# Kernel optimization log

Hardware: AMD Instinct MI355X
Metric: run time of the kernel (lower is better)

## Reference

```python
import jax, jax.numpy as jnp
import numpy as np

WS = 7        # window_size
SHIFT = 3     # shift_size
HEADS = 12
EMBED = 384


def _relative_position_index(ws: int) -> np.ndarray:
    coords = np.stack(np.meshgrid(np.arange(ws), np.arange(ws), indexing='ij'))  # [2,ws,ws]
    flat = coords.reshape(2, -1)                                                 # [2,ws*ws]
    rel = flat[:, :, None] - flat[:, None, :]                                     # [2,N,N]
    rel = rel.transpose(1, 2, 0)
    rel[:, :, 0] += ws - 1
    rel[:, :, 1] += ws - 1
    rel[:, :, 0] *= 2 * ws - 1
    return rel.sum(-1)  # [ws*ws, ws*ws]


def setup_inputs() -> dict:
    key = jax.random.key(0)
    ks = jax.random.split(key, 6)
    B, H, W, C = 32, 56, 56, EMBED
    x = jax.random.normal(ks[0], (B, H * W, C), dtype=jnp.float32)
    s = 0.02
    qkv_w = jax.random.normal(ks[1], (C, 3 * C), dtype=jnp.float32) * s
    qkv_b = jnp.zeros((3 * C,), dtype=jnp.float32)
    proj_w = jax.random.normal(ks[2], (C, C), dtype=jnp.float32) * s
    proj_b = jnp.zeros((C,), dtype=jnp.float32)
    rel_bias_table = jax.random.normal(ks[3], ((2 * WS - 1) ** 2, HEADS), dtype=jnp.float32) * s
    return {"x": x, "qkv_w": qkv_w, "qkv_b": qkv_b, "proj_w": proj_w,
            "proj_b": proj_b, "rel_bias_table": rel_bias_table, "H": H, "W": W}


def reference(x, qkv_w, qkv_b, proj_w, proj_b, rel_bias_table, H, W):
    B, L, C = x.shape
    hd = C // HEADS
    scale = hd ** (-0.5)
    ws = WS
    x = x.reshape(B, H, W, C)
    # pad to multiples of window size (static python ints)
    pad_r = (ws - W % ws) % ws
    pad_b_ = (ws - H % ws) % ws
    if pad_r or pad_b_:
        x = jnp.pad(x, ((0, 0), (0, pad_b_), (0, pad_r), (0, 0)))
    Hp, Wp = H + pad_b_, W + pad_r
    # cyclic shift
    if SHIFT > 0:
        x = jnp.roll(x, shift=(-SHIFT, -SHIFT), axis=(1, 2))
    # window partition -> [nW, ws*ws, C]
    nh, nw = Hp // ws, Wp // ws
    xw = x.reshape(B, nh, ws, nw, ws, C).transpose(0, 1, 3, 2, 4, 5).reshape(-1, ws * ws, C)
    # qkv projection
    qkv = xw @ qkv_w + qkv_b                               # [nW, N, 3C]
    qkv = qkv.reshape(-1, ws * ws, 3, HEADS, hd).transpose(2, 0, 3, 1, 4)
    q, k, v = qkv[0], qkv[1], qkv[2]                        # [nW, heads, N, hd]
    attn = jnp.einsum('whnd,whmd->whnm', q, k) * scale
    rpi = jnp.asarray(_relative_position_index(ws))         # [N, N] static
    bias = rel_bias_table[rpi.reshape(-1)].reshape(ws * ws, ws * ws, HEADS)
    attn = attn + bias.transpose(2, 0, 1)[None]             # [1, heads, N, N]
    attn = jax.nn.softmax(attn, axis=-1)
    out = jnp.einsum('whnm,whmd->whnd', attn, v)            # [nW, heads, N, hd]
    out = out.transpose(0, 2, 1, 3).reshape(-1, ws, ws, C)
    # merge windows
    out = out.reshape(B, nh, nw, ws, ws, C).transpose(0, 1, 3, 2, 4, 5).reshape(B, Hp, Wp, C)
    if SHIFT > 0:
        out = jnp.roll(out, shift=(SHIFT, SHIFT), axis=(1, 2))
    if pad_r or pad_b_:
        out = out[:, :H, :W, :]
    out = out.reshape(B, H * W, C)
    return out @ proj_w + proj_b
```

## Files before the change

### kernel.cpp

```cpp
#include <hip/hip_runtime.h>


typedef __attribute__((ext_vector_type(8))) short short8;
typedef __attribute__((ext_vector_type(4))) float floatx4;

#define CDIM  384
#define QKVN  1152
#define MROWS 100352
#define LROW  3136

static constexpr size_t QKV_ELEMS = 38535168ull;
static constexpr size_t OFF_Q    = 0;
static constexpr size_t OFF_K    = OFF_Q  + QKV_ELEMS * 2 + 4096;
static constexpr size_t OFF_V    = OFF_K  + QKV_ELEMS * 2 + 4096;
static constexpr size_t OFF_AO   = OFF_V  + QKV_ELEMS * 2 + 4096;
static constexpr size_t OFF_WQ   = OFF_AO + (size_t)MROWS * CDIM * 2 + 4096;
static constexpr size_t OFF_WP   = OFF_WQ + (size_t)QKVN * CDIM * 2 + 256;
static constexpr size_t OFF_BIAS = OFF_WP + (size_t)CDIM * CDIM * 2 + 256;

__device__ __forceinline__ unsigned short f2bf(float f) {
  unsigned int u = __float_as_uint(f);
  unsigned int lsb = (u >> 16) & 1u;
  u += 0x7fffu + lsb;
  return (unsigned short)(u >> 16);
}

__device__ __forceinline__ void gl2lds16(const void* g, void* l) {
  __builtin_amdgcn_global_load_lds(
      (const __attribute__((address_space(1))) unsigned int*)g,
      (__attribute__((address_space(3))) unsigned int*)l, 16, 0, 0);
}

__global__ __launch_bounds__(256) void prep_kernel(
    const float* __restrict__ x, const float* __restrict__ qkv_w,
    const float* __restrict__ proj_w, const float* __restrict__ rbt,
    char* __restrict__ ws) {
  unsigned short* Wq = (unsigned short*)(ws + OFF_WQ);
  unsigned short* Wp = (unsigned short*)(ws + OFF_WP);
  unsigned short* XB = (unsigned short*)(ws + OFF_AO);
  float* biasp = (float*)(ws + OFF_BIAS);
  const int tid = blockIdx.x * blockDim.x + threadIdx.x;
  const int stride = gridDim.x * blockDim.x;
  for (int idx = tid; idx < QKVN * CDIM; idx += stride) {
    int n = idx / CDIM, k = idx - n * CDIM;
    Wq[idx] = f2bf(qkv_w[(size_t)k * QKVN + n]);
  }
  for (int idx = tid; idx < CDIM * CDIM; idx += stride) {
    int n = idx / CDIM, k = idx - n * CDIM;
    Wp[idx] = f2bf(proj_w[(size_t)k * CDIM + n]);
  }
  for (int idx = tid; idx < 12 * 64 * 64; idx += stride) {
    int h = idx / 4096;
    int rem = idx - h * 4096;
    int lane = rem / 64;
    int e = rem - lane * 64;
    int fm = e >> 4, fn = (e >> 2) & 3, r = e & 3;
    int row = fm * 16 + (lane >> 4) * 4 + r;
    int col = fn * 16 + (lane & 15);
    float v = -1e30f;
    if (row < 49 && col < 49) {
      int i = row / 7, j = row - i * 7;
      int k2 = col / 7, l2 = col - k2 * 7;
      int rpi = (i - k2 + 6) * 13 + (j - l2 + 6);
      v = rbt[rpi * 12 + h];
    }
    biasp[idx] = v;
  }
  const size_t n8 = (size_t)MROWS * CDIM / 8;
  for (size_t idx = tid; idx < n8; idx += stride) {
    const float4* s = (const float4*)(x + idx * 8);
    float4 f0 = s[0], f1 = s[1];
    uint4 o;
    o.x = (unsigned)f2bf(f0.x) | ((unsigned)f2bf(f0.y) << 16);
    o.y = (unsigned)f2bf(f0.z) | ((unsigned)f2bf(f0.w) << 16);
    o.z = (unsigned)f2bf(f1.x) | ((unsigned)f2bf(f1.y) << 16);
    o.w = (unsigned)f2bf(f1.z) | ((unsigned)f2bf(f1.w) << 16);
    ((uint4*)XB)[idx] = o;
  }
}

__global__ __launch_bounds__(256) void qkv_gemm(
    const float* __restrict__ qkv_b, char* __restrict__ ws) {
  __shared__ unsigned short As[128][32];
  __shared__ unsigned short Bs[128][32];
  const unsigned short* XB = (const unsigned short*)(ws + OFF_AO);
  const unsigned short* Wq = (const unsigned short*)(ws + OFF_WQ);
  unsigned short* Qb = (unsigned short*)(ws + OFF_Q);
  unsigned short* Kb = (unsigned short*)(ws + OFF_K);
  unsigned short* Vb = (unsigned short*)(ws + OFF_V);
  const int L = blockIdx.x;
  const int xcd = L & 7, slot = L >> 3;
  const int g9 = slot / 9;
  const int m0 = (g9 * 8 + xcd) * 128;
  const int n0 = (slot - g9 * 9) * 128;
  const int t = threadIdx.x;
  const int lane = t & 63, li = lane & 15, qd = lane >> 4;
  const int wv = t >> 6, wm = wv >> 1, wn = wv & 1;
  const int ld_r = lane >> 2;
  const int ld_c = (lane & 3) * 8;
  const unsigned short* agp = XB + (size_t)(m0 + wv * 32 + ld_r) * CDIM + ld_c;
  const unsigned short* bgp = Wq + (size_t)(n0 + wv * 32 + ld_r) * CDIM + ld_c;
  floatx4 acc[4][4] = {};
  for (int k0 = 0; k0 < CDIM; k0 += 32) {
    gl2lds16(agp + k0,             &As[wv * 32][0]);
    gl2lds16(agp + k0 + 16 * CDIM, &As[wv * 32 + 16][0]);
    gl2lds16(bgp + k0,             &Bs[wv * 32][0]);
    gl2lds16(bgp + k0 + 16 * CDIM, &Bs[wv * 32 + 16][0]);
    __syncthreads();
    short8 a[4], b[4];
#pragma unroll
    for (int f = 0; f < 4; f++)
      a[f] = *(const short8*)&As[wm * 64 + f * 16 + li][qd * 8];
#pragma unroll
    for (int f = 0; f < 4; f++)
      b[f] = *(const short8*)&Bs[wn * 64 + f * 16 + li][qd * 8];
#pragma unroll
    for (int i = 0; i < 4; i++)
#pragma unroll
      for (int j = 0; j < 4; j++)
        acc[i][j] = __builtin_amdgcn_mfma_f32_16x16x32_bf16(a[i], b[j], acc[i][j], 0, 0, 0);
    __syncthreads();
  }
  const int which = n0 / CDIM;
  unsigned short* dst = which == 0 ? Qb : (which == 1 ? Kb : Vb);
  const float mul = (which == 0) ? 0.17677669529663689f : 1.0f;
#pragma unroll
  for (int i = 0; i < 4; i++) {
    int winr[4], nidxr[4];
#pragma unroll
    for (int r = 0; r < 4; r++) {
      int m = m0 + wm * 64 + i * 16 + qd * 4 + r;
      int b_ = m / LROW, l = m - b_ * LROW;
      int y = l / 56, xx = l - y * 56;
      int yr = y + 53; if (yr >= 56) yr -= 56;
      int xr = xx + 53; if (xr >= 56) xr -= 56;
      winr[r] = b_ * 64 + (yr / 7) * 8 + (xr / 7);
      nidxr[r] = (yr % 7) * 7 + (xr % 7);
    }
#pragma unroll
    for (int j = 0; j < 4; j++) {
      int c = n0 + wn * 64 + j * 16 + li;
      int cc = c - which * CDIM;
      int head = cc >> 5, d = cc & 31;
      float bval = qkv_b[c];
#pragma unroll
      for (int r = 0; r < 4; r++) {
        size_t off = ((size_t)(winr[r] * 12 + head) * 49 + nidxr[r]) * 32 + d;
        dst[off] = f2bf((acc[i][j][r] + bval) * mul);
      }
    }
  }
}

__global__ __launch_bounds__(256) void attn_kernel(char* __restrict__ ws) {
  __shared__ unsigned short SMEM[4][64 * 72];
  const int win = blockIdx.x;
  const int t = threadIdx.x, wv = t >> 6, lane = t & 63;
  const int h = blockIdx.y * 4 + wv;
  const int li = lane & 15, qd = lane >> 4;
  unsigned short* Sm = &SMEM[wv][0];
  const size_t whoff = (size_t)(win * 12 + h) * 49 * 32;
  const unsigned short* Qb = (const unsigned short*)(ws + OFF_Q) + whoff;
  const unsigned short* Kb = (const unsigned short*)(ws + OFF_K) + whoff;
  const unsigned short* Vb = (const unsigned short*)(ws + OFF_V) + whoff;
  const float* biasp = (const float*)(ws + OFF_BIAS) + ((size_t)h * 64 + lane) * 64;

  {
    const uint2* vsrc = (const uint2*)Vb;
    for (int idx = lane; idx < 392; idx += 64) {
      uint2 d = vsrc[idx];
      unsigned short* p = Sm + (idx >> 3) * 34 + (idx & 7) * 4;
      *(unsigned int*)p = d.x;
      *(unsigned int*)(p + 2) = d.y;
    }
    for (int idx = lane; idx < 120; idx += 64) {
      unsigned short* p = Sm + (49 + (idx >> 3)) * 34 + (idx & 7) * 4;
      *(unsigned int*)p = 0;
      *(unsigned int*)(p + 2) = 0;
    }
  }

  short8 qa[4], kb4[4];
#pragma unroll
  for (int f = 0; f < 4; f++) {
    qa[f] = *(const short8*)(Qb + (f * 16 + li) * 32 + qd * 8);
    kb4[f] = *(const short8*)(Kb + (f * 16 + li) * 32 + qd * 8);
  }
  floatx4 s[4][4] = {};
#pragma unroll
  for (int i = 0; i < 4; i++)
#pragma unroll
    for (int j = 0; j < 4; j++)
      s[i][j] = __builtin_amdgcn_mfma_f32_16x16x32_bf16(qa[i], kb4[j], s[i][j], 0, 0, 0);

  short8 vb[2][2];
#pragma unroll
  for (int ss = 0; ss < 2; ss++)
#pragma unroll
    for (int nf = 0; nf < 2; nf++) {
      short8 tmp;
#pragma unroll
      for (int j = 0; j < 8; j++)
        tmp[j] = (short)Sm[(ss * 32 + qd * 8 + j) * 34 + nf * 16 + li];
      vb[ss][nf] = tmp;
    }

  float rsum[4][4];
#pragma unroll
  for (int fm = 0; fm < 4; fm++) {
#pragma unroll
    for (int fn = 0; fn < 4; fn++) {
      floatx4 bv = *(const floatx4*)(biasp + (fm * 4 + fn) * 4);
#pragma unroll
      for (int r = 0; r < 4; r++)
        s[fm][fn][r] = __expf(s[fm][fn][r] + bv[r]);
    }
#pragma unroll
    for (int r = 0; r < 4; r++) {
      float v = s[fm][0][r] + s[fm][1][r] + s[fm][2][r] + s[fm][3][r];
      v += __shfl_xor(v, 1);
      v += __shfl_xor(v, 2);
      v += __shfl_xor(v, 4);
      v += __shfl_xor(v, 8);
      rsum[fm][r] = v;
    }
#pragma unroll
    for (int fn = 0; fn < 4; fn++)
#pragma unroll
      for (int r = 0; r < 4; r++)
        Sm[(fm * 16 + qd * 4 + r) * 72 + fn * 16 + li] = f2bf(s[fm][fn][r]);
  }

  floatx4 o[4][2] = {};
#pragma unroll
  for (int fm = 0; fm < 4; fm++)
#pragma unroll
    for (int ss = 0; ss < 2; ss++) {
      short8 pa = *(const short8*)&Sm[(fm * 16 + li) * 72 + ss * 32 + qd * 8];
#pragma unroll
      for (int nf = 0; nf < 2; nf++)
        o[fm][nf] = __builtin_amdgcn_mfma_f32_16x16x32_bf16(pa, vb[ss][nf], o[fm][nf], 0, 0, 0);
    }

  unsigned short* AO = (unsigned short*)(ws + OFF_AO);
  const int b_ = win >> 6, wrem = win & 63, wy = wrem >> 3, wx = wrem & 7;
#pragma unroll
  for (int fm = 0; fm < 4; fm++)
#pragma unroll
    for (int r = 0; r < 4; r++) {
      int n = fm * 16 + qd * 4 + r;
      if (n >= 49) continue;
      float inv = 1.0f / rsum[fm][r];
      int i_ = n / 7, j_ = n - i_ * 7;
      int y = wy * 7 + i_ + 3;  if (y >= 56) y -= 56;
      int xx = wx * 7 + j_ + 3; if (xx >= 56) xx -= 56;
      size_t base = ((size_t)b_ * LROW + y * 56 + xx) * CDIM + h * 32;
#pragma unroll
      for (int nf = 0; nf < 2; nf++)
        AO[base + nf * 16 + li] = f2bf(o[fm][nf][r] * inv);
    }
}

__global__ __launch_bounds__(256) void proj_gemm(
    const float* __restrict__ proj_b, char* __restrict__ ws,
    float* __restrict__ out) {
  __shared__ unsigned short As[128][32];
  __shared__ unsigned short Bs[128][32];
  const unsigned short* AO = (const unsigned short*)(ws + OFF_AO);
  const unsigned short* Wp = (const unsigned short*)(ws + OFF_WP);
  const int L = blockIdx.x;
  const int xcd = L & 7, slot = L >> 3;
  const int g3 = slot / 3;
  const int m0 = (g3 * 8 + xcd) * 128;
  const int n0 = (slot - g3 * 3) * 128;
  const int t = threadIdx.x;
  const int lane = t & 63, li = lane & 15, qd = lane >> 4;
  const int wv = t >> 6, wm = wv >> 1, wn = wv & 1;
  const int ld_r = lane >> 2;
  const int ld_c = (lane & 3) * 8;
  const unsigned short* agp = AO + (size_t)(m0 + wv * 32 + ld_r) * CDIM + ld_c;
  const unsigned short* bgp = Wp + (size_t)(n0 + wv * 32 + ld_r) * CDIM + ld_c;
  floatx4 acc[4][4] = {};
  for (int k0 = 0; k0 < CDIM; k0 += 32) {
    gl2lds16(agp + k0,             &As[wv * 32][0]);
    gl2lds16(agp + k0 + 16 * CDIM, &As[wv * 32 + 16][0]);
    gl2lds16(bgp + k0,             &Bs[wv * 32][0]);
    gl2lds16(bgp + k0 + 16 * CDIM, &Bs[wv * 32 + 16][0]);
    __syncthreads();
    short8 a[4], b[4];
#pragma unroll
    for (int f = 0; f < 4; f++)
      a[f] = *(const short8*)&As[wm * 64 + f * 16 + li][qd * 8];
#pragma unroll
    for (int f = 0; f < 4; f++)
      b[f] = *(const short8*)&Bs[wn * 64 + f * 16 + li][qd * 8];
#pragma unroll
    for (int i = 0; i < 4; i++)
#pragma unroll
      for (int j = 0; j < 4; j++)
        acc[i][j] = __builtin_amdgcn_mfma_f32_16x16x32_bf16(a[i], b[j], acc[i][j], 0, 0, 0);
    __syncthreads();
  }
#pragma unroll
  for (int i = 0; i < 4; i++)
#pragma unroll
    for (int j = 0; j < 4; j++) {
      int c = n0 + wn * 64 + j * 16 + li;
      float bv = proj_b[c];
#pragma unroll
      for (int r = 0; r < 4; r++) {
        int m = m0 + wm * 64 + i * 16 + qd * 4 + r;
        out[(size_t)m * CDIM + c] = acc[i][j][r] + bv;
      }
    }
}

extern "C" void kernel_launch(void* const* d_in, const int* in_sizes, int n_in,
                              void* d_out, int out_size, void* d_ws, size_t ws_size,
                              hipStream_t stream) {
  const float* x      = (const float*)d_in[0];
  const float* qkv_w  = (const float*)d_in[1];
  const float* qkv_b  = (const float*)d_in[2];
  const float* proj_w = (const float*)d_in[3];
  const float* proj_b = (const float*)d_in[4];
  const float* rbt    = (const float*)d_in[5];
  char* ws = (char*)d_ws;
  float* out = (float*)d_out;

  prep_kernel<<<2048, 256, 0, stream>>>(x, qkv_w, proj_w, rbt, ws);
  qkv_gemm<<<7056, 256, 0, stream>>>(qkv_b, ws);
  attn_kernel<<<dim3(2048, 3), 256, 0, stream>>>(ws);
  proj_gemm<<<2352, 256, 0, stream>>>(proj_b, ws, out);
}
```

Before: 611.6 us.

## Double-buffer LDS tiles in both GEMMs and precompute window-scatter offsets

Both the QKV and projection GEMMs now use two LDS buffers and issue the global-to-LDS loads for the next K tile before computing the current one, so load latency can overlap MFMA work. A lookup table of per-row window scatter offsets is built in the prep kernel and read in the QKV epilogue, replacing the integer divides and mods. This doubles LDS use per block, which may lower occupancy. The global_load_lds writes are not waited on explicitly before the barrier, so correctness relies on the sync implying vmcnt drain.

```diff
diff --git a/kernel.cpp b/kernel.cpp
--- a/kernel.cpp
+++ b/kernel.cpp
@@ -17,6 +17,7 @@
 static constexpr size_t OFF_WQ   = OFF_AO + (size_t)MROWS * CDIM * 2 + 4096;
 static constexpr size_t OFF_WP   = OFF_WQ + (size_t)QKVN * CDIM * 2 + 256;
 static constexpr size_t OFF_BIAS = OFF_WP + (size_t)CDIM * CDIM * 2 + 256;
+static constexpr size_t OFF_LUT  = OFF_BIAS + (size_t)12 * 64 * 64 * 4 + 256;
 
 __device__ __forceinline__ unsigned short f2bf(float f) {
   unsigned int u = __float_as_uint(f);
@@ -39,6 +40,7 @@
   unsigned short* Wp = (unsigned short*)(ws + OFF_WP);
   unsigned short* XB = (unsigned short*)(ws + OFF_AO);
   float* biasp = (float*)(ws + OFF_BIAS);
+  int* lut = (int*)(ws + OFF_LUT);
   const int tid = blockIdx.x * blockDim.x + threadIdx.x;
   const int stride = gridDim.x * blockDim.x;
   for (int idx = tid; idx < QKVN * CDIM; idx += stride) {
@@ -66,6 +68,15 @@
     }
     biasp[idx] = v;
   }
+  for (int idx = tid; idx < MROWS; idx += stride) {
+    int b_ = idx / LROW, l = idx - b_ * LROW;
+    int y = l / 56, xx = l - y * 56;
+    int yr = y + 53; if (yr >= 56) yr -= 56;
+    int xr = xx + 53; if (xr >= 56) xr -= 56;
+    int win = b_ * 64 + (yr / 7) * 8 + (xr / 7);
+    int nidx = (yr % 7) * 7 + (xr % 7);
+    lut[idx] = win * 18816 + nidx * 32;
+  }
   const size_t n8 = (size_t)MROWS * CDIM / 8;
   for (size_t idx = tid; idx < n8; idx += stride) {
     const float4* s = (const float4*)(x + idx * 8);
@@ -81,13 +92,14 @@
 
 __global__ __launch_bounds__(256) void qkv_gemm(
     const float* __restrict__ qkv_b, char* __restrict__ ws) {
-  __shared__ unsigned short As[128][32];
-  __shared__ unsigned short Bs[128][32];
+  __shared__ unsigned short As[2][128][32];
+  __shared__ unsigned short Bs[2][128][32];
   const unsigned short* XB = (const unsigned short*)(ws + OFF_AO);
   const unsigned short* Wq = (const unsigned short*)(ws + OFF_WQ);
   unsigned short* Qb = (unsigned short*)(ws + OFF_Q);
   unsigned short* Kb = (unsigned short*)(ws + OFF_K);
   unsigned short* Vb = (unsigned short*)(ws + OFF_V);
+  const int* lut = (const int*)(ws + OFF_LUT);
   const int L = blockIdx.x;
   const int xcd = L & 7, slot = L >> 3;
   const int g9 = slot / 9;
@@ -100,20 +112,28 @@
   const int ld_c = (lane & 3) * 8;
   const unsigned short* agp = XB + (size_t)(m0 + wv * 32 + ld_r) * CDIM + ld_c;
   const unsigned short* bgp = Wq + (size_t)(n0 + wv * 32 + ld_r) * CDIM + ld_c;
+
+#define QSTAGE(buf, k0)                                          \
+  do {                                                           \
+    gl2lds16(agp + (k0),             &As[buf][wv * 32][0]);      \
+    gl2lds16(agp + (k0) + 16 * CDIM, &As[buf][wv * 32 + 16][0]); \
+    gl2lds16(bgp + (k0),             &Bs[buf][wv * 32][0]);      \
+    gl2lds16(bgp + (k0) + 16 * CDIM, &Bs[buf][wv * 32 + 16][0]); \
+  } while (0)
+
   floatx4 acc[4][4] = {};
-  for (int k0 = 0; k0 < CDIM; k0 += 32) {
-    gl2lds16(agp + k0,             &As[wv * 32][0]);
-    gl2lds16(agp + k0 + 16 * CDIM, &As[wv * 32 + 16][0]);
-    gl2lds16(bgp + k0,             &Bs[wv * 32][0]);
-    gl2lds16(bgp + k0 + 16 * CDIM, &Bs[wv * 32 + 16][0]);
-    __syncthreads();
+  QSTAGE(0, 0);
+  __syncthreads();
+  for (int kt = 0; kt < 12; ++kt) {
+    const int cur = kt & 1;
+    if (kt < 11) QSTAGE(cur ^ 1, (kt + 1) * 32);
     short8 a[4], b[4];
 #pragma unroll
     for (int f = 0; f < 4; f++)
-      a[f] = *(const short8*)&As[wm * 64 + f * 16 + li][qd * 8];
+      a[f] = *(const short8*)&As[cur][wm * 64 + f * 16 + li][qd * 8];
 #pragma unroll
     for (int f = 0; f < 4; f++)
-      b[f] = *(const short8*)&Bs[wn * 64 + f * 16 + li][qd * 8];
+      b[f] = *(const short8*)&Bs[cur][wn * 64 + f * 16 + li][qd * 8];
 #pragma unroll
     for (int i = 0; i < 4; i++)
 #pragma unroll
@@ -121,31 +141,27 @@
         acc[i][j] = __builtin_amdgcn_mfma_f32_16x16x32_bf16(a[i], b[j], acc[i][j], 0, 0, 0);
     __syncthreads();
   }
+#undef QSTAGE
+
   const int which = n0 / CDIM;
   unsigned short* dst = which == 0 ? Qb : (which == 1 ? Kb : Vb);
   const float mul = (which == 0) ? 0.17677669529663689f : 1.0f;
 #pragma unroll
   for (int i = 0; i < 4; i++) {
-    int winr[4], nidxr[4];
-#pragma unroll
-    for (int r = 0; r < 4; r++) {
-      int m = m0 + wm * 64 + i * 16 + qd * 4 + r;
-      int b_ = m / LROW, l = m - b_ * LROW;
-      int y = l / 56, xx = l - y * 56;
-      int yr = y + 53; if (yr >= 56) yr -= 56;
-      int xr = xx + 53; if (xr >= 56) xr -= 56;
-      winr[r] = b_ * 64 + (yr / 7) * 8 + (xr / 7);
-      nidxr[r] = (yr % 7) * 7 + (xr % 7);
-    }
+    int lbase[4];
+#pragma unroll
+    for (int r = 0; r < 4; r++)
+      lbase[r] = lut[m0 + wm * 64 + i * 16 + qd * 4 + r];
 #pragma unroll
     for (int j = 0; j < 4; j++) {
       int c = n0 + wn * 64 + j * 16 + li;
       int cc = c - which * CDIM;
       int head = cc >> 5, d = cc & 31;
+      int hd_off = head * 1568 + d;
       float bval = qkv_b[c];
 #pragma unroll
       for (int r = 0; r < 4; r++) {
-        size_t off = ((size_t)(winr[r] * 12 + head) * 49 + nidxr[r]) * 32 + d;
+        size_t off = (size_t)(lbase[r] + hd_off);
         dst[off] = f2bf((acc[i][j][r] + bval) * mul);
       }
     }
@@ -264,8 +280,8 @@
 __global__ __launch_bounds__(256) void proj_gemm(
     const float* __restrict__ proj_b, char* __restrict__ ws,
     float* __restrict__ out) {
-  __shared__ unsigned short As[128][32];
-  __shared__ unsigned short Bs[128][32];
+  __shared__ unsigned short As[2][128][32];
+  __shared__ unsigned short Bs[2][128][32];
   const unsigned short* AO = (const unsigned short*)(ws + OFF_AO);
   const unsigned short* Wp = (const unsigned short*)(ws + OFF_WP);
   const int L = blockIdx.x;
@@ -280,20 +296,28 @@
   const int ld_c = (lane & 3) * 8;
   const unsigned short* agp = AO + (size_t)(m0 + wv * 32 + ld_r) * CDIM + ld_c;
   const unsigned short* bgp = Wp + (size_t)(n0 + wv * 32 + ld_r) * CDIM + ld_c;
+
+#define PSTAGE(buf, k0)                                          \
+  do {                                                           \
+    gl2lds16(agp + (k0),             &As[buf][wv * 32][0]);      \
+    gl2lds16(agp + (k0) + 16 * CDIM, &As[buf][wv * 32 + 16][0]); \
+    gl2lds16(bgp + (k0),             &Bs[buf][wv * 32][0]);      \
+    gl2lds16(bgp + (k0) + 16 * CDIM, &Bs[buf][wv * 32 + 16][0]); \
+  } while (0)
+
   floatx4 acc[4][4] = {};
-  for (int k0 = 0; k0 < CDIM; k0 += 32) {
-    gl2lds16(agp + k0,             &As[wv * 32][0]);
-    gl2lds16(agp + k0 + 16 * CDIM, &As[wv * 32 + 16][0]);
-    gl2lds16(bgp + k0,             &Bs[wv * 32][0]);
-    gl2lds16(bgp + k0 + 16 * CDIM, &Bs[wv * 32 + 16][0]);
-    __syncthreads();
+  PSTAGE(0, 0);
+  __syncthreads();
+  for (int kt = 0; kt < 12; ++kt) {
+    const int cur = kt & 1;
+    if (kt < 11) PSTAGE(cur ^ 1, (kt + 1) * 32);
     short8 a[4], b[4];
 #pragma unroll
     for (int f = 0; f < 4; f++)
-      a[f] = *(const short8*)&As[wm * 64 + f * 16 + li][qd * 8];
+      a[f] = *(const short8*)&As[cur][wm * 64 + f * 16 + li][qd * 8];
 #pragma unroll
     for (int f = 0; f < 4; f++)
-      b[f] = *(const short8*)&Bs[wn * 64 + f * 16 + li][qd * 8];
+      b[f] = *(const short8*)&Bs[cur][wn * 64 + f * 16 + li][qd * 8];
 #pragma unroll
     for (int i = 0; i < 4; i++)
 #pragma unroll
@@ -301,6 +325,8 @@
         acc[i][j] = __builtin_amdgcn_mfma_f32_16x16x32_bf16(a[i], b[j], acc[i][j], 0, 0, 0);
     __syncthreads();
   }
+#undef PSTAGE
+
 #pragma unroll
   for (int i = 0; i < 4; i++)
 #pragma unroll
```

Result: no change. 615.2 us (+0.6%).

## Store QKV row-major via LDS staging and gather windows in attention

Applied to the files above, without the earlier changes.

The QKV GEMM epilogue now stages bf16 results in shared memory and writes full 16-byte vectors into a row-major [M, 1152] buffer. Before, it scattered 2-byte stores into a per-window, per-head layout. The attention kernel takes over the cyclic-shift and window indexing: it gathers Q/K rows directly from the row-major buffer and transposes V into LDS so V fragments load as vectors. This trades badly coalesced stores for gathered reads of 64-byte row segments in the attention kernel.

```diff
diff --git a/kernel.cpp b/kernel.cpp
--- a/kernel.cpp
+++ b/kernel.cpp
@@ -81,13 +81,12 @@
 
 __global__ __launch_bounds__(256) void qkv_gemm(
     const float* __restrict__ qkv_b, char* __restrict__ ws) {
-  __shared__ unsigned short As[128][32];
-  __shared__ unsigned short Bs[128][32];
+  __shared__ unsigned short SMEM[8192];
+  unsigned short (*As)[32] = (unsigned short (*)[32])(&SMEM[0]);
+  unsigned short (*Bs)[32] = (unsigned short (*)[32])(&SMEM[4096]);
   const unsigned short* XB = (const unsigned short*)(ws + OFF_AO);
   const unsigned short* Wq = (const unsigned short*)(ws + OFF_WQ);
-  unsigned short* Qb = (unsigned short*)(ws + OFF_Q);
-  unsigned short* Kb = (unsigned short*)(ws + OFF_K);
-  unsigned short* Vb = (unsigned short*)(ws + OFF_V);
+  unsigned short* QKVm = (unsigned short*)(ws + OFF_Q);
   const int L = blockIdx.x;
   const int xcd = L & 7, slot = L >> 3;
   const int g9 = slot / 9;
@@ -100,6 +99,7 @@
   const int ld_c = (lane & 3) * 8;
   const unsigned short* agp = XB + (size_t)(m0 + wv * 32 + ld_r) * CDIM + ld_c;
   const unsigned short* bgp = Wq + (size_t)(n0 + wv * 32 + ld_r) * CDIM + ld_c;
+
   floatx4 acc[4][4] = {};
   for (int k0 = 0; k0 < CDIM; k0 += 32) {
     gl2lds16(agp + k0,             &As[wv * 32][0]);
@@ -121,34 +121,37 @@
         acc[i][j] = __builtin_amdgcn_mfma_f32_16x16x32_bf16(a[i], b[j], acc[i][j], 0, 0, 0);
     __syncthreads();
   }
-  const int which = n0 / CDIM;
-  unsigned short* dst = which == 0 ? Qb : (which == 1 ? Kb : Vb);
-  const float mul = (which == 0) ? 0.17677669529663689f : 1.0f;
-#pragma unroll
-  for (int i = 0; i < 4; i++) {
-    int winr[4], nidxr[4];
-#pragma unroll
-    for (int r = 0; r < 4; r++) {
-      int m = m0 + wm * 64 + i * 16 + qd * 4 + r;
-      int b_ = m / LROW, l = m - b_ * LROW;
-      int y = l / 56, xx = l - y * 56;
-      int yr = y + 53; if (yr >= 56) yr -= 56;
-      int xr = xx + 53; if (xr >= 56) xr -= 56;
-      winr[r] = b_ * 64 + (yr / 7) * 8 + (xr / 7);
-      nidxr[r] = (yr % 7) * 7 + (xr % 7);
-    }
-#pragma unroll
-    for (int j = 0; j < 4; j++) {
-      int c = n0 + wn * 64 + j * 16 + li;
-      int cc = c - which * CDIM;
-      int head = cc >> 5, d = cc & 31;
-      float bval = qkv_b[c];
-#pragma unroll
-      for (int r = 0; r < 4; r++) {
-        size_t off = ((size_t)(winr[r] * 12 + head) * 49 + nidxr[r]) * 32 + d;
-        dst[off] = f2bf((acc[i][j][r] + bval) * mul);
-      }
-    }
+
+  const float mul = (n0 < 384) ? 0.17677669529663689f : 1.0f;
+  float bvals[4];
+#pragma unroll
+  for (int j = 0; j < 4; j++)
+    bvals[j] = qkv_b[n0 + wn * 64 + j * 16 + li];
+
+#pragma unroll
+  for (int half = 0; half < 2; half++) {
+    if (wn == half) {
+#pragma unroll
+      for (int i = 0; i < 4; i++)
+#pragma unroll
+        for (int j = 0; j < 4; j++)
+#pragma unroll
+          for (int r = 0; r < 4; r++) {
+            int row = wm * 64 + i * 16 + qd * 4 + r;
+            int col = j * 16 + li;
+            SMEM[row * 64 + col] = f2bf((acc[i][j][r] + bvals[j]) * mul);
+          }
+    }
+    __syncthreads();
+    {
+      int r = t >> 1;
+      int c0 = (t & 1) * 32;
+      const uint4* src = (const uint4*)&SMEM[r * 64 + c0];
+      uint4* dst = (uint4*)(QKVm + (size_t)(m0 + r) * QKVN + n0 + half * 64 + c0);
+      uint4 v0 = src[0], v1 = src[1], v2 = src[2], v3 = src[3];
+      dst[0] = v0; dst[1] = v1; dst[2] = v2; dst[3] = v3;
+    }
+    __syncthreads();
   }
 }
 
@@ -159,33 +162,38 @@
   const int h = blockIdx.y * 4 + wv;
   const int li = lane & 15, qd = lane >> 4;
   unsigned short* Sm = &SMEM[wv][0];
-  const size_t whoff = (size_t)(win * 12 + h) * 49 * 32;
-  const unsigned short* Qb = (const unsigned short*)(ws + OFF_Q) + whoff;
-  const unsigned short* Kb = (const unsigned short*)(ws + OFF_K) + whoff;
-  const unsigned short* Vb = (const unsigned short*)(ws + OFF_V) + whoff;
+  const unsigned short* QKVm = (const unsigned short*)(ws + OFF_Q);
   const float* biasp = (const float*)(ws + OFF_BIAS) + ((size_t)h * 64 + lane) * 64;
-
-  {
-    const uint2* vsrc = (const uint2*)Vb;
-    for (int idx = lane; idx < 392; idx += 64) {
-      uint2 d = vsrc[idx];
-      unsigned short* p = Sm + (idx >> 3) * 34 + (idx & 7) * 4;
-      *(unsigned int*)p = d.x;
-      *(unsigned int*)(p + 2) = d.y;
-    }
-    for (int idx = lane; idx < 120; idx += 64) {
-      unsigned short* p = Sm + (49 + (idx >> 3)) * 34 + (idx & 7) * 4;
-      *(unsigned int*)p = 0;
-      *(unsigned int*)(p + 2) = 0;
-    }
-  }
+  const int b_ = win >> 6, wrem = win & 63, wy = wrem >> 3, wx = wrem & 7;
+  const int qoff = h * 32, koff = 384 + h * 32, voff = 768 + h * 32;
+
+  auto msrc_of = [&](int n) -> int {
+    int i_ = n / 7, j_ = n - i_ * 7;
+    int y = wy * 7 + i_ + 3;  if (y >= 56) y -= 56;
+    int xx = wx * 7 + j_ + 3; if (xx >= 56) xx -= 56;
+    return b_ * LROW + y * 56 + xx;
+  };
 
   short8 qa[4], kb4[4];
 #pragma unroll
   for (int f = 0; f < 4; f++) {
-    qa[f] = *(const short8*)(Qb + (f * 16 + li) * 32 + qd * 8);
-    kb4[f] = *(const short8*)(Kb + (f * 16 + li) * 32 + qd * 8);
-  }
+    const unsigned short* rowp = QKVm + (size_t)msrc_of(f * 16 + li) * QKVN;
+    qa[f]  = *(const short8*)(rowp + qoff + qd * 8);
+    kb4[f] = *(const short8*)(rowp + koff + qd * 8);
+  }
+
+  for (int idx = lane; idx < 512; idx += 64)
+    Sm[(idx >> 4) * 72 + 48 + (idx & 15)] = 0;
+  for (int idx = lane; idx < 392; idx += 64) {
+    int row = idx >> 3, d0 = (idx & 7) * 4;
+    const unsigned short* rowp = QKVm + (size_t)msrc_of(row) * QKVN + voff;
+    uint2 dv = *(const uint2*)(rowp + d0);
+    Sm[(d0 + 0) * 72 + row] = (unsigned short)(dv.x & 0xffff);
+    Sm[(d0 + 1) * 72 + row] = (unsigned short)(dv.x >> 16);
+    Sm[(d0 + 2) * 72 + row] = (unsigned short)(dv.y & 0xffff);
+    Sm[(d0 + 3) * 72 + row] = (unsigned short)(dv.y >> 16);
+  }
+
   floatx4 s[4][4] = {};
 #pragma unroll
   for (int i = 0; i < 4; i++)
@@ -197,13 +205,8 @@
 #pragma unroll
   for (int ss = 0; ss < 2; ss++)
 #pragma unroll
-    for (int nf = 0; nf < 2; nf++) {
-      short8 tmp;
-#pragma unroll
-      for (int j = 0; j < 8; j++)
-        tmp[j] = (short)Sm[(ss * 32 + qd * 8 + j) * 34 + nf * 16 + li];
-      vb[ss][nf] = tmp;
-    }
+    for (int nf = 0; nf < 2; nf++)
+      vb[ss][nf] = *(const short8*)&Sm[(nf * 16 + li) * 72 + ss * 32 + qd * 8];
 
   float rsum[4][4];
 #pragma unroll
@@ -243,7 +246,6 @@
     }
 
   unsigned short* AO = (unsigned short*)(ws + OFF_AO);
-  const int b_ = win >> 6, wrem = win & 63, wy = wrem >> 3, wx = wrem & 7;
 #pragma unroll
   for (int fm = 0; fm < 4; fm++)
 #pragma unroll
@@ -251,10 +253,7 @@
       int n = fm * 16 + qd * 4 + r;
       if (n >= 49) continue;
       float inv = 1.0f / rsum[fm][r];
-      int i_ = n / 7, j_ = n - i_ * 7;
-      int y = wy * 7 + i_ + 3;  if (y >= 56) y -= 56;
-      int xx = wx * 7 + j_ + 3; if (xx >= 56) xx -= 56;
-      size_t base = ((size_t)b_ * LROW + y * 56 + xx) * CDIM + h * 32;
+      size_t base = (size_t)msrc_of(n) * CDIM + h * 32;
 #pragma unroll
       for (int nf = 0; nf < 2; nf++)
         AO[base + nf * 16 + li] = f2bf(o[fm][nf][r] * inv);
```

After: 659.7 us. +7.9%, slower.
